# Optimization experiments

Hardware: AMD Instinct MI355X
Metric: run time of the kernel (lower is better)

## Reference

```python
import jax, jax.numpy as jnp
import numpy as np

B = 32768
W = 7            # window_size (fixed: classifier head outputs 7*2 -> view(B, 7, 2))
F = 80           # per-frame feature size
WF = W * F       # window_feature_size = 560
EH = 512         # encoder_hidden_size
EO = 512         # encoder_output_size
H = 512          # core_hidden_size
NUM_STEPS = 7
EPS = 1e-5

def _linear(x, w, b):
    return x @ w.T + b

def _bn(x, g, bt, m, v):
    # BatchNorm1d in eval mode (running stats)
    return (x - m) * g / jnp.sqrt(v + EPS) + bt

def _ln(x, g, b):
    mu = x.mean(-1, keepdims=True)
    var = x.var(-1, keepdims=True)
    return (x - mu) / jnp.sqrt(var + EPS) * g + b

def setup_inputs():
    key = jax.random.key(0)
    ks = iter(jax.random.split(key, 40))
    def rn(shape, s=0.05):
        return jax.random.normal(next(ks), shape, dtype=jnp.float32) * s
    def rv(shape):
        return jax.random.uniform(next(ks), shape, dtype=jnp.float32) + 0.5
    return {
        'features': jax.random.normal(next(ks), (B, W, F), dtype=jnp.float32),
        'dec_w': rn((W, H)), 'dec_b': rn((W,)),
        'dec_bn_g': rv((W,)), 'dec_bn_b': rn((W,)), 'dec_bn_m': rn((W,)), 'dec_bn_v': rv((W,)),
        'ea1_w': rn((EH, W)), 'ea1_b': rn((EH,)),
        'ea1_bn_g': rv((EH,)), 'ea1_bn_b': rn((EH,)), 'ea1_bn_m': rn((EH,)), 'ea1_bn_v': rv((EH,)),
        'ea2_w': rn((EO, EH)), 'ea2_b': rn((EO,)),
        'ea2_bn_g': rv((EO,)), 'ea2_bn_b': rn((EO,)), 'ea2_bn_m': rn((EO,)), 'ea2_bn_v': rv((EO,)),
        'ei1_w': rn((EH, WF)), 'ei1_b': rn((EH,)),
        'ei1_bn_g': rv((EH,)), 'ei1_bn_b': rn((EH,)), 'ei1_bn_m': rn((EH,)), 'ei1_bn_v': rv((EH,)),
        'ei2_w': rn((EO, EH)), 'ei2_b': rn((EO,)),
        'ei2_bn_g': rv((EO,)), 'ei2_bn_b': rn((EO,)), 'ei2_bn_m': rn((EO,)), 'ei2_bn_v': rv((EO,)),
        'w_ih': rn((4 * H, EO)), 'w_hh': rn((4 * H, H)), 'b_ih': rn((4 * H,)), 'b_hh': rn((4 * H,)),
        'ln_g': rv((H,)), 'ln_b': rn((H,)),
        'cls_w': rn((2 * W, H)), 'cls_b': rn((2 * W,)),
    }

def _forward(features, dec_w, dec_b, dec_bn_g, dec_bn_b, dec_bn_m, dec_bn_v,
             ea1_w, ea1_b, ea1_bn_g, ea1_bn_b, ea1_bn_m, ea1_bn_v,
             ea2_w, ea2_b, ea2_bn_g, ea2_bn_b, ea2_bn_m, ea2_bn_v,
             ei1_w, ei1_b, ei1_bn_g, ei1_bn_b, ei1_bn_m, ei1_bn_v,
             ei2_w, ei2_b, ei2_bn_g, ei2_bn_b, ei2_bn_m, ei2_bn_v,
             w_ih, w_hh, b_ih, b_hh, ln_g, ln_b, cls_w, cls_b):
    Bsz = features.shape[0]

    def encoder(att):
        # attention branch: Linear -> BN -> ReLU -> Linear -> BN
        a = jax.nn.relu(_bn(_linear(att, ea1_w, ea1_b), ea1_bn_g, ea1_bn_b, ea1_bn_m, ea1_bn_v))
        a = _bn(_linear(a, ea2_w, ea2_b), ea2_bn_g, ea2_bn_b, ea2_bn_m, ea2_bn_v)
        # attended-input branch on flattened (features * att)
        ai = (features * att[:, :, None]).reshape(Bsz, WF)
        x = jax.nn.relu(_bn(_linear(ai, ei1_w, ei1_b), ei1_bn_g, ei1_bn_b, ei1_bn_m, ei1_bn_v))
        x = _bn(_linear(x, ei2_w, ei2_b), ei2_bn_g, ei2_bn_b, ei2_bn_m, ei2_bn_v)
        return jax.nn.relu(a + x)

    def lstm_step(x, h, c):
        gates = x @ w_ih.T + b_ih + h @ w_hh.T + b_hh  # [B, 4H], torch gate order i,f,g,o
        i, f, g, o = jnp.split(gates, 4, axis=-1)
        c = jax.nn.sigmoid(f) * c + jax.nn.sigmoid(i) * jnp.tanh(g)
        h = jax.nn.sigmoid(o) * jnp.tanh(c)
        return h, c

    # initial pass: uniform attention, zero LSTM state (state=None -> no LN)
    att0 = jnp.full((Bsz, W), 1.0 / W, dtype=features.dtype)
    h, c = lstm_step(encoder(att0), jnp.zeros((Bsz, H), features.dtype), jnp.zeros((Bsz, H), features.dtype))

    def body(carry, _):
        h, c = carry
        # decoder: Linear -> BN -> smooth softmax
        logits = _bn(_linear(h, dec_w, dec_b), dec_bn_g, dec_bn_b, dec_bn_m, dec_bn_v)
        s = jax.nn.sigmoid(logits)
        att = s / s.sum(-1, keepdims=True)
        agg = encoder(att)
        hn, cn = lstm_step(agg, _ln(h, ln_g, ln_b), _ln(c, ln_g, ln_b))
        return (hn, cn), None

    (h, c), _ = jax.lax.scan(body, (h, c), None, length=NUM_STEPS)
    out = _linear(h, cls_w, cls_b).reshape(Bsz, W, 2)
    return jax.nn.log_softmax(out, axis=2)

def reference(features, dec_w, dec_b, dec_bn_g, dec_bn_b, dec_bn_m, dec_bn_v,
              ea1_w, ea1_b, ea1_bn_g, ea1_bn_b, ea1_bn_m, ea1_bn_v,
              ea2_w, ea2_b, ea2_bn_g, ea2_bn_b, ea2_bn_m, ea2_bn_v,
              ei1_w, ei1_b, ei1_bn_g, ei1_bn_b, ei1_bn_m, ei1_bn_v,
              ei2_w, ei2_b, ei2_bn_g, ei2_bn_b, ei2_bn_m, ei2_bn_v,
              w_ih, w_hh, b_ih, b_hh, ln_g, ln_b, cls_w, cls_b):
    return _forward(features, dec_w, dec_b, dec_bn_g, dec_bn_b, dec_bn_m, dec_bn_v,
                    ea1_w, ea1_b, ea1_bn_g, ea1_bn_b, ea1_bn_m, ea1_bn_v,
                    ea2_w, ea2_b, ea2_bn_g, ea2_bn_b, ea2_bn_m, ea2_bn_v,
                    ei1_w, ei1_b, ei1_bn_g, ei1_bn_b, ei1_bn_m, ei1_bn_v,
                    ei2_w, ei2_b, ei2_bn_g, ei2_bn_b, ei2_bn_m, ei2_bn_v,
                    w_ih, w_hh, b_ih, b_hh, ln_g, ln_b, cls_w, cls_b)
```

## Files before the change

kernel.cpp:

```cpp
#include <hip/hip_runtime.h>
#include <cstdint>
#include <cstddef>

#define BSZ 32768
#define WN 7
#define WF 560
#define K1P 576
#define EPS 1e-5f

typedef __attribute__((ext_vector_type(8))) short bf16x8;
typedef __attribute__((ext_vector_type(4))) float f32x4;

__device__ __forceinline__ float b2f(short s) {
  union { float f; unsigned u; } x; x.u = ((unsigned)(unsigned short)s) << 16; return x.f;
}
__device__ __forceinline__ short f2b(float f) {
  union { float f; unsigned u; } x; x.f = f;
  unsigned r = x.u + 0x7fffu + ((x.u >> 16) & 1u);
  return (short)(r >> 16);
}
__device__ __forceinline__ float sigf(float x) { return 1.0f / (1.0f + __expf(-x)); }
__device__ __forceinline__ float ftanh(float x) {
  float t = __expf(-2.0f * fabsf(x));
  float r = (1.0f - t) / (1.0f + t);
  return copysignf(r, x);
}

__device__ __forceinline__ void async_copy16(const short* g, short* l) {
  __builtin_amdgcn_global_load_lds((const __attribute__((address_space(1))) unsigned*)g,
                                   (__attribute__((address_space(3))) unsigned*)l, 16, 0, 0);
}


__global__ void fold_small_k(const float* __restrict__ dec_w, const float* __restrict__ dec_b,
                             const float* __restrict__ dec_g, const float* __restrict__ dec_bt,
                             const float* __restrict__ dec_m, const float* __restrict__ dec_v,
                             const float* __restrict__ ea1_w, const float* __restrict__ ea1_b,
                             const float* __restrict__ ea1_g, const float* __restrict__ ea1_bt,
                             const float* __restrict__ ea1_m, const float* __restrict__ ea1_v,
                             float* __restrict__ decwf, float* __restrict__ decb8,
                             float* __restrict__ ea1f)
{
  int t = blockIdx.x * 256 + threadIdx.x;
  if (t < 7 * 512) {
    int w = t >> 9;
    float s = dec_g[w] * rsqrtf(dec_v[w] + EPS);
    decwf[t] = dec_w[t] * s;
  }
  if (t < 8) {
    if (t < 7) {
      float s = dec_g[t] * rsqrtf(dec_v[t] + EPS);
      decb8[t] = (dec_b[t] - dec_m[t]) * s + dec_bt[t];
    } else decb8[t] = 0.0f;
  }
  if (t < 512) {
    float s = ea1_g[t] * rsqrtf(ea1_v[t] + EPS);
    #pragma unroll
    for (int w = 0; w < 7; ++w) ea1f[t * 8 + w] = ea1_w[t * 7 + w] * s;
    ea1f[t * 8 + 7] = (ea1_b[t] - ea1_m[t]) * s + ea1_bt[t];
  }
}

__global__ void fold_ei1_k(const float* __restrict__ w, const float* __restrict__ b,
                           const float* __restrict__ g, const float* __restrict__ bt,
                           const float* __restrict__ m, const float* __restrict__ v,
                           short* __restrict__ ei1f, float* __restrict__ bias1)
{
  int idx = blockIdx.x * 256 + threadIdx.x;
  int n = idx / K1P, k = idx % K1P;
  float s = g[n] * rsqrtf(v[n] + EPS);
  ei1f[idx] = (k < WF) ? f2b(w[n * WF + k] * s) : (short)0;
  if (k == 0) bias1[n] = (b[n] - m[n]) * s + bt[n];
}

__global__ void fold_w2_k(const float* __restrict__ wi, const float* __restrict__ bi,
                          const float* __restrict__ gi, const float* __restrict__ bti,
                          const float* __restrict__ mi, const float* __restrict__ vi,
                          const float* __restrict__ wa, const float* __restrict__ ba,
                          const float* __restrict__ ga, const float* __restrict__ bta,
                          const float* __restrict__ ma, const float* __restrict__ va,
                          short* __restrict__ W2, float* __restrict__ bias2)
{
  int idx = blockIdx.x * 256 + threadIdx.x;
  int n = idx >> 10, k = idx & 1023;
  float si = gi[n] * rsqrtf(vi[n] + EPS);
  float sa = ga[n] * rsqrtf(va[n] + EPS);
  float val = (k < 512) ? wi[n * 512 + k] * si : wa[n * 512 + (k - 512)] * sa;
  W2[idx] = f2b(val);
  if (k == 0)
    bias2[n] = (bi[n] - mi[n]) * si + bti[n] + (ba[n] - ma[n]) * sa + bta[n];
}

__global__ void fold_wg_k(const float* __restrict__ w_ih, const float* __restrict__ w_hh,
                          const float* __restrict__ b_ih, const float* __restrict__ b_hh,
                          short* __restrict__ Wg, float* __restrict__ biasg)
{
  int idx = blockIdx.x * 256 + threadIdx.x;
  int c = idx >> 10, k = idx & 1023;
  int g = (c >> 4) & 3;
  int u = (c >> 6) * 16 + (c & 15);
  int r = g * 512 + u;
  float val = (k < 512) ? w_ih[r * 512 + k] : w_hh[r * 512 + (k - 512)];
  Wg[idx] = f2b(val);
  if (k == 0) biasg[c] = b_ih[r] + b_hh[r];
}

__global__ __launch_bounds__(512)
void attln_k(const float* __restrict__ hbuf, const float* __restrict__ cbuf,
             const float* __restrict__ decwf, const float* __restrict__ decb8,
             const float* __restrict__ ea1f,
             const float* __restrict__ ln_g, const float* __restrict__ ln_b,
             const float* __restrict__ feat,
             short* __restrict__ ghA, short* __restrict__ c_ln,
             short* __restrict__ xa, short* __restrict__ ai, int init)
{
  const int lane = threadIdx.x & 63;
  const int b = blockIdx.x * 8 + (threadIdx.x >> 6);
  float av[WN];
  if (init) {
    const float c7 = 1.0f / 7.0f;
    #pragma unroll
    for (int w = 0; w < WN; ++w) av[w] = c7;
    int4 z = make_int4(0, 0, 0, 0);
    *(int4*)&ghA[b * 1024 + 512 + lane * 8] = z;
    *(int4*)&c_ln[b * 512 + lane * 8] = z;
  } else {
    float hl[8];
    const float* hp = hbuf + (size_t)b * 512 + lane * 8;
    *(float4*)&hl[0] = *(const float4*)hp;
    *(float4*)&hl[4] = *(const float4*)(hp + 4);
    float s = 0.f, s2 = 0.f;
    #pragma unroll
    for (int e = 0; e < 8; ++e) { s += hl[e]; s2 += hl[e] * hl[e]; }
    float p[WN];
    #pragma unroll
    for (int w = 0; w < WN; ++w) {
      const float* dw = decwf + w * 512 + lane * 8;
      float4 w0 = *(const float4*)dw, w1 = *(const float4*)(dw + 4);
      p[w] = hl[0] * w0.x + hl[1] * w0.y + hl[2] * w0.z + hl[3] * w0.w
           + hl[4] * w1.x + hl[5] * w1.y + hl[6] * w1.z + hl[7] * w1.w;
    }
    #pragma unroll
    for (int o = 32; o > 0; o >>= 1) {
      s  += __shfl_xor(s, o);
      s2 += __shfl_xor(s2, o);
      #pragma unroll
      for (int w = 0; w < WN; ++w) p[w] += __shfl_xor(p[w], o);
    }
    float mu = s * (1.0f / 512.0f);
    float var = s2 * (1.0f / 512.0f) - mu * mu;
    float rstd = rsqrtf(var + EPS);
    float ssum = 0.f;
    #pragma unroll
    for (int w = 0; w < WN; ++w) { float sg = sigf(p[w] + decb8[w]); av[w] = sg; ssum += sg; }
    float inv = 1.0f / ssum;
    #pragma unroll
    for (int w = 0; w < WN; ++w) av[w] *= inv;
    short o8[8];
    #pragma unroll
    for (int e = 0; e < 8; ++e) {
      int i = lane * 8 + e;
      o8[e] = f2b((hl[e] - mu) * rstd * ln_g[i] + ln_b[i]);
    }
    *(int4*)&ghA[b * 1024 + 512 + lane * 8] = *(int4*)o8;
    float cl[8];
    const float* cp = cbuf + (size_t)b * 512 + lane * 8;
    *(float4*)&cl[0] = *(const float4*)cp;
    *(float4*)&cl[4] = *(const float4*)(cp + 4);
    float cs = 0.f, cs2 = 0.f;
    #pragma unroll
    for (int e = 0; e < 8; ++e) { cs += cl[e]; cs2 += cl[e] * cl[e]; }
    #pragma unroll
    for (int o = 32; o > 0; o >>= 1) {
      cs  += __shfl_xor(cs, o);
      cs2 += __shfl_xor(cs2, o);
    }
    float cmu = cs * (1.0f / 512.0f);
    float cvar = cs2 * (1.0f / 512.0f) - cmu * cmu;
    float crstd = rsqrtf(cvar + EPS);
    #pragma unroll
    for (int e = 0; e < 8; ++e) {
      int i = lane * 8 + e;
      o8[e] = f2b((cl[e] - cmu) * crstd * ln_g[i] + ln_b[i]);
    }
    *(int4*)&c_ln[b * 512 + lane * 8] = *(int4*)o8;
  }
  short a8[8];
  #pragma unroll
  for (int e = 0; e < 8; ++e) {
    int n = lane * 8 + e;
    const float* wr = ea1f + n * 8;
    float4 w0 = *(const float4*)wr, w1 = *(const float4*)(wr + 4);
    float v = w1.w
            + av[0] * w0.x + av[1] * w0.y + av[2] * w0.z + av[3] * w0.w
            + av[4] * w1.x + av[5] * w1.y + av[6] * w1.z;
    a8[e] = f2b(fmaxf(v, 0.0f));
  }
  *(int4*)&xa[b * 1024 + 512 + lane * 8] = *(int4*)a8;
  const float* fr = feat + (size_t)b * WF;
  short* air = ai + (size_t)b * K1P;
  #pragma unroll
  for (int rr = 0; rr < 2; ++rr) {
    int c8 = lane + rr * 64;
    if (c8 < 72) {
      int k = c8 * 8;
      short s8[8];
      if (k < WF) {
        int window = c8 / 10;
        float a = av[0];
        #pragma unroll
        for (int w = 1; w < WN; ++w) a = (window == w) ? av[w] : a;
        float4 f0 = *(const float4*)(fr + k);
        float4 f1 = *(const float4*)(fr + k + 4);
        s8[0] = f2b(f0.x * a); s8[1] = f2b(f0.y * a); s8[2] = f2b(f0.z * a); s8[3] = f2b(f0.w * a);
        s8[4] = f2b(f1.x * a); s8[5] = f2b(f1.y * a); s8[6] = f2b(f1.z * a); s8[7] = f2b(f1.w * a);
      } else {
        #pragma unroll
        for (int e = 0; e < 8; ++e) s8[e] = 0;
      }
      *(int4*)&air[k] = *(int4*)s8;
    }
  }
}

#define STAGE128(SRC, LD, K0, S) do {                                          \
    _Pragma("unroll")                                                          \
    for (int r_ = 0; r_ < 4; ++r_) {                                           \
      int idx_ = r_ * 256 + t;                                                 \
      int row_ = idx_ >> 3, dcol_ = (idx_ & 7) * 8;                            \
      int scol_ = dcol_ ^ ((row_ & 7) << 3);                                   \
      async_copy16(SRC + (size_t)row_ * (LD) + (K0) + scol_, &S[idx_ * 8]);    \
    }                                                                          \
  } while (0)

#define READ_FRAG(S, ROW, KS) \
  (*(const bf16x8*)&S[(ROW) * 64 + (((KS)) ^ (((ROW) & 7) << 3))])

__global__ __launch_bounds__(256)
void gemm_bt_k(const short* __restrict__ A, int lda,
               const short* __restrict__ Wt, int K,
               const float* __restrict__ bias,
               short* __restrict__ C, int ldc)
{
  const int bswz = blockIdx.x;
  const int xcd = bswz & 7, slot = bswz >> 3;
  const int m0 = (xcd + 8 * (slot >> 2)) * 128;
  const int n0 = (slot & 3) * 128;
  __shared__ short sA[128 * 64];
  __shared__ short sB[128 * 64];
  const int t = threadIdx.x;
  const int wv = t >> 6, lane = t & 63;
  const int wm = (wv & 1) * 64, wn = (wv >> 1) * 64;
  const int lr = lane & 15, lk = (lane >> 4) * 8;

  f32x4 acc[4][4] = {};
  const short* Ab = A + (size_t)m0 * lda;
  const short* Wb = Wt + (size_t)n0 * K;

  for (int k0 = 0; k0 < K; k0 += 64) {
    STAGE128(Ab, lda, k0, sA);
    STAGE128(Wb, K, k0, sB);
    __syncthreads();
    #pragma unroll
    for (int ks = 0; ks < 64; ks += 32) {
      bf16x8 af[4], bfr[4];
      #pragma unroll
      for (int i = 0; i < 4; ++i) af[i]  = READ_FRAG(sA, wm + i * 16 + lr, ks + lk);
      #pragma unroll
      for (int j = 0; j < 4; ++j) bfr[j] = READ_FRAG(sB, wn + j * 16 + lr, ks + lk);
      #pragma unroll
      for (int i = 0; i < 4; ++i)
        #pragma unroll
        for (int j = 0; j < 4; ++j)
          acc[i][j] = __builtin_amdgcn_mfma_f32_16x16x32_bf16(af[i], bfr[j], acc[i][j], 0, 0, 0);
    }
    __syncthreads();
  }
  #pragma unroll
  for (int j = 0; j < 4; ++j) {
    int col = n0 + wn + j * 16 + lr;
    float bs = bias[col];
    #pragma unroll
    for (int i = 0; i < 4; ++i) {
      int rbase = m0 + wm + i * 16 + (lane >> 4) * 4;
      #pragma unroll
      for (int e = 0; e < 4; ++e) {
        float v = acc[i][j][e] + bs;
        C[(size_t)(rbase + e) * ldc + col] = f2b(fmaxf(v, 0.0f));
      }
    }
  }
}


#define GS_STAGE(g) do {                                                             \
    short* dA_ = &sA[((g) & 1) * 16384];                                             \
    short* dB_ = &sB[((g) & 1) * 16384];                                             \
    _Pragma("unroll")                                                                \
    for (int q_ = 0; q_ < 4; ++q_) {                                                 \
      int idx_ = q_ * 512 + t;                                                       \
      int row_ = idx_ >> 3, ds_ = idx_ & 7;                                          \
      int sc_ = (ds_ ^ (row_ & 7)) * 8;                                              \
      async_copy16(A + (size_t)(m0 + row_) * 1024 + (g) * 64 + sc_, dA_ + idx_ * 8); \
    }                                                                                \
    _Pragma("unroll")                                                                \
    for (int q_ = 0; q_ < 4; ++q_) {                                                 \
      int idx_ = q_ * 512 + t;                                                       \
      int row_ = idx_ >> 3, ds_ = idx_ & 7;                                          \
      int sc_ = (ds_ ^ (row_ & 7)) * 8;                                              \
      async_copy16(Wg + (size_t)(n0 + row_) * 1024 + (g) * 64 + sc_, dB_ + idx_ * 8);\
    }                                                                                \
  } while (0)

#define GS_COMPUTE(g) do {                                                           \
    const short* bA_ = &sA[((g) & 1) * 16384];                                       \
    const short* bB_ = &sB[((g) & 1) * 16384];                                       \
    _Pragma("unroll")                                                                \
    for (int ks_ = 0; ks_ < 2; ++ks_) {                                              \
      bf16x8 af_[4], bf_[8];                                                         \
      _Pragma("unroll")                                                              \
      for (int mf_ = 0; mf_ < 4; ++mf_) {                                            \
        int row_ = wm * 64 + mf_ * 16 + lr;                                          \
        af_[mf_] = *(const bf16x8*)&bA_[row_ * 64 + (((ks_ * 4 + hi) ^ (row_ & 7)) * 8)]; \
      }                                                                              \
      _Pragma("unroll")                                                              \
      for (int nf_ = 0; nf_ < 8; ++nf_) {                                            \
        int row_ = wn * 128 + nf_ * 16 + lr;                                         \
        bf_[nf_] = *(const bf16x8*)&bB_[row_ * 64 + (((ks_ * 4 + hi) ^ (row_ & 7)) * 8)]; \
      }                                                                              \
      __builtin_amdgcn_s_setprio(1);                                                 \
      _Pragma("unroll")                                                              \
      for (int mf_ = 0; mf_ < 4; ++mf_)                                              \
        _Pragma("unroll")                                                            \
        for (int nf_ = 0; nf_ < 8; ++nf_)                                            \
          acc[mf_][nf_] = __builtin_amdgcn_mfma_f32_16x16x32_bf16(af_[mf_], bf_[nf_], acc[mf_][nf_], 0, 0, 0); \
      __builtin_amdgcn_s_setprio(0);                                                 \
    }                                                                                \
  } while (0)

__global__ __launch_bounds__(512, 2)
void gates_k(const short* __restrict__ A,
             const short* __restrict__ Wg,
             const float* __restrict__ biasg,
             const short* __restrict__ c_ln,
             float* __restrict__ hbuf, float* __restrict__ cbuf)
{
  __shared__ short sA[2 * 256 * 64];
  __shared__ short sB[2 * 256 * 64];
  const int m0 = blockIdx.x * 256;
  const int n0 = blockIdx.y * 256;
  const int t = threadIdx.x;
  const int wid = t >> 6, lane = t & 63;
  const int wm = wid >> 1, wn = wid & 1;
  const int lr = lane & 15, hi = lane >> 4;

  f32x4 acc[4][8] = {};

  GS_STAGE(0);
  asm volatile("s_waitcnt vmcnt(0)" ::: "memory");
  __builtin_amdgcn_s_barrier();

  #pragma unroll
  for (int g = 0; g < 16; ++g) {
    if (g + 1 < 16) GS_STAGE(g + 1);
    GS_COMPUTE(g);
    if (g + 1 < 16) {
      asm volatile("s_waitcnt vmcnt(0) lgkmcnt(0)" ::: "memory");
      __builtin_amdgcn_s_barrier();
    }
  }

  #pragma unroll
  for (int grp = 0; grp < 2; ++grp) {
    const int cb = n0 + wn * 128 + grp * 64;
    const int u = ((cb >> 6)) * 16 + lr;
    const float bi_ = biasg[cb + 0 * 16 + lr];
    const float bf2 = biasg[cb + 1 * 16 + lr];
    const float bg_ = biasg[cb + 2 * 16 + lr];
    const float bo_ = biasg[cb + 3 * 16 + lr];
    #pragma unroll
    for (int mf = 0; mf < 4; ++mf) {
      int rbase = m0 + wm * 64 + mf * 16 + hi * 4;
      #pragma unroll
      for (int e = 0; e < 4; ++e) {
        int row = rbase + e;
        float iv = sigf(acc[mf][grp * 4 + 0][e] + bi_);
        float fv = sigf(acc[mf][grp * 4 + 1][e] + bf2);
        float gv = ftanh(acc[mf][grp * 4 + 2][e] + bg_);
        float ov = sigf(acc[mf][grp * 4 + 3][e] + bo_);
        float cold = b2f(c_ln[(size_t)row * 512 + u]);
        float cc = fv * cold + iv * gv;
        hbuf[(size_t)row * 512 + u] = ov * ftanh(cc);
        cbuf[(size_t)row * 512 + u] = cc;
      }
    }
  }
}

__global__ __launch_bounds__(512)
void cls_k(const float* __restrict__ hbuf, const float* __restrict__ cw,
           const float* __restrict__ cb, float* __restrict__ out)
{
  const int lane = threadIdx.x & 63;
  const int b = blockIdx.x * 8 + (threadIdx.x >> 6);
  float hl[8];
  const float* hp = hbuf + (size_t)b * 512 + lane * 8;
  *(float4*)&hl[0] = *(const float4*)hp;
  *(float4*)&hl[4] = *(const float4*)(hp + 4);
  float p[14];
  #pragma unroll
  for (int tcol = 0; tcol < 14; ++tcol) {
    const float* wr = cw + tcol * 512 + lane * 8;
    float4 w0 = *(const float4*)wr, w1 = *(const float4*)(wr + 4);
    p[tcol] = hl[0] * w0.x + hl[1] * w0.y + hl[2] * w0.z + hl[3] * w0.w
            + hl[4] * w1.x + hl[5] * w1.y + hl[6] * w1.z + hl[7] * w1.w;
  }
  #pragma unroll
  for (int o = 32; o > 0; o >>= 1)
    #pragma unroll
    for (int tcol = 0; tcol < 14; ++tcol) p[tcol] += __shfl_xor(p[tcol], o);
  if (lane < 14) {
    float z = cb[lane];
    #pragma unroll
    for (int tcol = 0; tcol < 14; ++tcol) if (lane == tcol) z += p[tcol];
    float zp = __shfl_xor(z, 1);
    float m = fmaxf(z, zp);
    float l = m + __logf(__expf(z - m) + __expf(zp - m));
    out[(size_t)b * 14 + lane] = z - l;
  }
}


extern "C" void kernel_launch(void* const* d_in, const int* in_sizes, int n_in,
                              void* d_out, int out_size, void* d_ws, size_t ws_size,
                              hipStream_t stream)
{
  const float* features = (const float*)d_in[0];
  const float* dec_w    = (const float*)d_in[1];
  const float* dec_b    = (const float*)d_in[2];
  const float* dec_bn_g = (const float*)d_in[3];
  const float* dec_bn_b = (const float*)d_in[4];
  const float* dec_bn_m = (const float*)d_in[5];
  const float* dec_bn_v = (const float*)d_in[6];
  const float* ea1_w    = (const float*)d_in[7];
  const float* ea1_b    = (const float*)d_in[8];
  const float* ea1_bn_g = (const float*)d_in[9];
  const float* ea1_bn_b = (const float*)d_in[10];
  const float* ea1_bn_m = (const float*)d_in[11];
  const float* ea1_bn_v = (const float*)d_in[12];
  const float* ea2_w    = (const float*)d_in[13];
  const float* ea2_b    = (const float*)d_in[14];
  const float* ea2_bn_g = (const float*)d_in[15];
  const float* ea2_bn_b = (const float*)d_in[16];
  const float* ea2_bn_m = (const float*)d_in[17];
  const float* ea2_bn_v = (const float*)d_in[18];
  const float* ei1_w    = (const float*)d_in[19];
  const float* ei1_b    = (const float*)d_in[20];
  const float* ei1_bn_g = (const float*)d_in[21];
  const float* ei1_bn_b = (const float*)d_in[22];
  const float* ei1_bn_m = (const float*)d_in[23];
  const float* ei1_bn_v = (const float*)d_in[24];
  const float* ei2_w    = (const float*)d_in[25];
  const float* ei2_b    = (const float*)d_in[26];
  const float* ei2_bn_g = (const float*)d_in[27];
  const float* ei2_bn_b = (const float*)d_in[28];
  const float* ei2_bn_m = (const float*)d_in[29];
  const float* ei2_bn_v = (const float*)d_in[30];
  const float* w_ih     = (const float*)d_in[31];
  const float* w_hh     = (const float*)d_in[32];
  const float* b_ih     = (const float*)d_in[33];
  const float* b_hh     = (const float*)d_in[34];
  const float* ln_g     = (const float*)d_in[35];
  const float* ln_b     = (const float*)d_in[36];
  const float* cls_w    = (const float*)d_in[37];
  const float* cls_b    = (const float*)d_in[38];
  (void)in_sizes; (void)n_in; (void)out_size;

  int chunk = BSZ;
  while (chunk > 2048 && (size_t)chunk * 10368 + (16u << 20) > ws_size) chunk >>= 1;

  char* ws = (char*)d_ws;
  size_t off = 0;
  auto carve = [&](size_t bytes) -> void* {
    void* p = ws + off;
    off += (bytes + 255) & ~(size_t)255;
    return p;
  };
  short* ei1f  = (short*)carve((size_t)512 * K1P * 2);
  float* bias1 = (float*)carve(512 * 4);
  short* W2    = (short*)carve((size_t)512 * 1024 * 2);
  float* bias2 = (float*)carve(512 * 4);
  short* Wg    = (short*)carve((size_t)2048 * 1024 * 2);
  float* biasg = (float*)carve(2048 * 4);
  float* decwf = (float*)carve(7 * 512 * 4);
  float* decb8 = (float*)carve(8 * 4);
  float* ea1f  = (float*)carve(512 * 8 * 4);
  float* hbuf  = (float*)carve((size_t)chunk * 512 * 4);
  float* cbuf  = (float*)carve((size_t)chunk * 512 * 4);
  short* ghA   = (short*)carve((size_t)chunk * 1024 * 2);
  short* xa    = (short*)carve((size_t)chunk * 1024 * 2);
  short* clnb  = (short*)carve((size_t)chunk * 512 * 2);
  short* ai    = (short*)carve((size_t)chunk * K1P * 2);

  fold_small_k<<<16, 256, 0, stream>>>(dec_w, dec_b, dec_bn_g, dec_bn_b, dec_bn_m, dec_bn_v,
                                       ea1_w, ea1_b, ea1_bn_g, ea1_bn_b, ea1_bn_m, ea1_bn_v,
                                       decwf, decb8, ea1f);
  fold_ei1_k<<<(512 * K1P) / 256, 256, 0, stream>>>(ei1_w, ei1_b, ei1_bn_g, ei1_bn_b,
                                                    ei1_bn_m, ei1_bn_v, ei1f, bias1);
  fold_w2_k<<<(512 * 1024) / 256, 256, 0, stream>>>(ei2_w, ei2_b, ei2_bn_g, ei2_bn_b, ei2_bn_m, ei2_bn_v,
                                                    ea2_w, ea2_b, ea2_bn_g, ea2_bn_b, ea2_bn_m, ea2_bn_v,
                                                    W2, bias2);
  fold_wg_k<<<(2048 * 1024) / 256, 256, 0, stream>>>(w_ih, w_hh, b_ih, b_hh, Wg, biasg);

  for (int base = 0; base < BSZ; base += chunk) {
    const float* featc = features + (size_t)base * WF;
    float* outc = (float*)d_out + (size_t)base * 14;
    for (int s = 0; s < 8; ++s) {
      attln_k<<<chunk / 8, 512, 0, stream>>>(hbuf, cbuf, decwf, decb8, ea1f, ln_g, ln_b,
                                             featc, ghA, clnb, xa, ai, (s == 0) ? 1 : 0);
      gemm_bt_k<<<(chunk / 128) * 4, 256, 0, stream>>>(ai, K1P, ei1f, K1P, bias1, xa, 1024);
      gemm_bt_k<<<(chunk / 128) * 4, 256, 0, stream>>>(xa, 1024, W2, 1024, bias2, ghA, 1024);
      gates_k<<<dim3(chunk / 256, 8), 512, 0, stream>>>(ghA, Wg, biasg, clnb, hbuf, cbuf);
    }
    cls_k<<<chunk / 8, 512, 0, stream>>>(hbuf, cls_w, cls_b, outc);
  }
}
```

Baseline: 2.765 ms.

## Interleave B-fragment LDS loads with MFMA quarters in gates GEMM loop

Restructures the gates GEMM inner loop so that each K-tile is computed in four N-quarters. B fragments for the next quarter are double-buffered in registers and loaded from LDS while the current quarter's MFMAs run, and extra barriers are inserted between quarters. The goal is to hide LDS read latency behind matrix-core work and to spread LDS traffic across waves. In exchange it adds barriers per tile, which can add sync overhead and register pressure.

```diff
diff --git a/kernel.cpp b/kernel.cpp
--- a/kernel.cpp
+++ b/kernel.cpp
@@ -312,29 +312,13 @@
     }                                                                                \
   } while (0)
 
-#define GS_COMPUTE(g) do {                                                           \
-    const short* bA_ = &sA[((g) & 1) * 16384];                                       \
-    const short* bB_ = &sB[((g) & 1) * 16384];                                       \
+#define GS_LOADB(BUF, DST, NQ) do {                                                  \
     _Pragma("unroll")                                                                \
-    for (int ks_ = 0; ks_ < 2; ++ks_) {                                              \
-      bf16x8 af_[4], bf_[8];                                                         \
+    for (int nfi_ = 0; nfi_ < 2; ++nfi_) {                                           \
+      int row_ = wn * 128 + (NQ) * 32 + nfi_ * 16 + lr;                              \
       _Pragma("unroll")                                                              \
-      for (int mf_ = 0; mf_ < 4; ++mf_) {                                            \
-        int row_ = wm * 64 + mf_ * 16 + lr;                                          \
-        af_[mf_] = *(const bf16x8*)&bA_[row_ * 64 + (((ks_ * 4 + hi) ^ (row_ & 7)) * 8)]; \
-      }                                                                              \
-      _Pragma("unroll")                                                              \
-      for (int nf_ = 0; nf_ < 8; ++nf_) {                                            \
-        int row_ = wn * 128 + nf_ * 16 + lr;                                         \
-        bf_[nf_] = *(const bf16x8*)&bB_[row_ * 64 + (((ks_ * 4 + hi) ^ (row_ & 7)) * 8)]; \
-      }                                                                              \
-      __builtin_amdgcn_s_setprio(1);                                                 \
-      _Pragma("unroll")                                                              \
-      for (int mf_ = 0; mf_ < 4; ++mf_)                                              \
-        _Pragma("unroll")                                                            \
-        for (int nf_ = 0; nf_ < 8; ++nf_)                                            \
-          acc[mf_][nf_] = __builtin_amdgcn_mfma_f32_16x16x32_bf16(af_[mf_], bf_[nf_], acc[mf_][nf_], 0, 0, 0); \
-      __builtin_amdgcn_s_setprio(0);                                                 \
+      for (int ks_ = 0; ks_ < 2; ++ks_)                                              \
+        DST[nfi_][ks_] = *(const bf16x8*)&BUF[row_ * 64 + (((ks_ * 4 + hi) ^ (row_ & 7)) * 8)]; \
     }                                                                                \
   } while (0)
 
@@ -362,12 +346,45 @@
 
   #pragma unroll
   for (int g = 0; g < 16; ++g) {
+    const short* bA_ = &sA[(g & 1) * 16384];
+    const short* bB_ = &sB[(g & 1) * 16384];
     if (g + 1 < 16) GS_STAGE(g + 1);
-    GS_COMPUTE(g);
-    if (g + 1 < 16) {
-      asm volatile("s_waitcnt vmcnt(0) lgkmcnt(0)" ::: "memory");
+
+    bf16x8 af_[4][2];
+    #pragma unroll
+    for (int mf_ = 0; mf_ < 4; ++mf_) {
+      int row_ = wm * 64 + mf_ * 16 + lr;
+      #pragma unroll
+      for (int ks_ = 0; ks_ < 2; ++ks_)
+        af_[mf_][ks_] = *(const bf16x8*)&bA_[row_ * 64 + (((ks_ * 4 + hi) ^ (row_ & 7)) * 8)];
+    }
+    bf16x8 b0[2][2], b1[2][2];
+    GS_LOADB(bB_, b0, 0);
+
+    #pragma unroll
+    for (int q = 0; q < 4; ++q) {
       __builtin_amdgcn_s_barrier();
-    }
+      __builtin_amdgcn_s_setprio(1);
+      #pragma unroll
+      for (int mf_ = 0; mf_ < 4; ++mf_)
+        #pragma unroll
+        for (int nfi_ = 0; nfi_ < 2; ++nfi_) {
+          if (q & 1) {
+            acc[mf_][q * 2 + nfi_] = __builtin_amdgcn_mfma_f32_16x16x32_bf16(af_[mf_][0], b1[nfi_][0], acc[mf_][q * 2 + nfi_], 0, 0, 0);
+            acc[mf_][q * 2 + nfi_] = __builtin_amdgcn_mfma_f32_16x16x32_bf16(af_[mf_][1], b1[nfi_][1], acc[mf_][q * 2 + nfi_], 0, 0, 0);
+          } else {
+            acc[mf_][q * 2 + nfi_] = __builtin_amdgcn_mfma_f32_16x16x32_bf16(af_[mf_][0], b0[nfi_][0], acc[mf_][q * 2 + nfi_], 0, 0, 0);
+            acc[mf_][q * 2 + nfi_] = __builtin_amdgcn_mfma_f32_16x16x32_bf16(af_[mf_][1], b0[nfi_][1], acc[mf_][q * 2 + nfi_], 0, 0, 0);
+          }
+        }
+      __builtin_amdgcn_s_setprio(0);
+      if (q == 0) GS_LOADB(bB_, b1, 1);
+      else if (q == 1) GS_LOADB(bB_, b0, 2);
+      else if (q == 2) GS_LOADB(bB_, b1, 3);
+      else if (g + 1 < 16)
+        asm volatile("s_waitcnt vmcnt(0)" ::: "memory");
+    }
+    __builtin_amdgcn_s_barrier();
   }
 
   #pragma unroll
```

Result: no change. 2.783 ms (+0.7%).

## Double-buffer LDS tiles in encoder GEMM to overlap loads with MFMA

Applied to the files above, without the earlier changes.

The encoder GEMM now uses two LDS buffers for A and B, issuing the async copies for the next K-tile before computing on the current one. It then waits on vmcnt and a barrier before the next iteration. The K trip count becomes a template parameter so the loop fully unrolls. The aim is to hide global-memory latency behind MFMA work. In exchange LDS use doubles to 64KB per block, which may reduce occupancy, and the unroll raises code size.

```diff
diff --git a/kernel.cpp b/kernel.cpp
--- a/kernel.cpp
+++ b/kernel.cpp
@@ -223,19 +223,30 @@
   }
 }
 
-#define STAGE128(SRC, LD, K0, S) do {                                          \
-    _Pragma("unroll")                                                          \
-    for (int r_ = 0; r_ < 4; ++r_) {                                           \
-      int idx_ = r_ * 256 + t;                                                 \
-      int row_ = idx_ >> 3, dcol_ = (idx_ & 7) * 8;                            \
-      int scol_ = dcol_ ^ ((row_ & 7) << 3);                                   \
-      async_copy16(SRC + (size_t)row_ * (LD) + (K0) + scol_, &S[idx_ * 8]);    \
-    }                                                                          \
+
+#define E_STAGE(g) do {                                                              \
+    short* dA_ = &sA[((g) & 1) * 8192];                                              \
+    short* dB_ = &sB[((g) & 1) * 8192];                                              \
+    _Pragma("unroll")                                                                \
+    for (int q_ = 0; q_ < 4; ++q_) {                                                 \
+      int idx_ = q_ * 256 + t;                                                       \
+      int row_ = idx_ >> 3, dcol_ = (idx_ & 7) * 8;                                  \
+      int scol_ = dcol_ ^ ((row_ & 7) << 3);                                         \
+      async_copy16(Ab + (size_t)row_ * lda + (g) * 64 + scol_, dA_ + idx_ * 8);      \
+    }                                                                                \
+    _Pragma("unroll")                                                                \
+    for (int q_ = 0; q_ < 4; ++q_) {                                                 \
+      int idx_ = q_ * 256 + t;                                                       \
+      int row_ = idx_ >> 3, dcol_ = (idx_ & 7) * 8;                                  \
+      int scol_ = dcol_ ^ ((row_ & 7) << 3);                                         \
+      async_copy16(Wb + (size_t)row_ * K + (g) * 64 + scol_, dB_ + idx_ * 8);        \
+    }                                                                                \
   } while (0)
 
-#define READ_FRAG(S, ROW, KS) \
-  (*(const bf16x8*)&S[(ROW) * 64 + (((KS)) ^ (((ROW) & 7) << 3))])
-
+#define READ_FRAGB(BASE, ROW, KS) \
+  (*(const bf16x8*)&BASE[(ROW) * 64 + (((KS)) ^ (((ROW) & 7) << 3))])
+
+template<int KT>
 __global__ __launch_bounds__(256)
 void gemm_bt_k(const short* __restrict__ A, int lda,
                const short* __restrict__ Wt, int K,
@@ -246,8 +257,8 @@
   const int xcd = bswz & 7, slot = bswz >> 3;
   const int m0 = (xcd + 8 * (slot >> 2)) * 128;
   const int n0 = (slot & 3) * 128;
-  __shared__ short sA[128 * 64];
-  __shared__ short sB[128 * 64];
+  __shared__ short sA[2 * 128 * 64];
+  __shared__ short sB[2 * 128 * 64];
   const int t = threadIdx.x;
   const int wv = t >> 6, lane = t & 63;
   const int wm = (wv & 1) * 64, wn = (wv >> 1) * 64;
@@ -257,24 +268,32 @@
   const short* Ab = A + (size_t)m0 * lda;
   const short* Wb = Wt + (size_t)n0 * K;
 
-  for (int k0 = 0; k0 < K; k0 += 64) {
-    STAGE128(Ab, lda, k0, sA);
-    STAGE128(Wb, K, k0, sB);
-    __syncthreads();
+  E_STAGE(0);
+  asm volatile("s_waitcnt vmcnt(0)" ::: "memory");
+  __builtin_amdgcn_s_barrier();
+
+  #pragma unroll
+  for (int g = 0; g < KT; ++g) {
+    const short* bA_ = &sA[(g & 1) * 8192];
+    const short* bB_ = &sB[(g & 1) * 8192];
+    if (g + 1 < KT) E_STAGE(g + 1);
     #pragma unroll
     for (int ks = 0; ks < 64; ks += 32) {
       bf16x8 af[4], bfr[4];
       #pragma unroll
-      for (int i = 0; i < 4; ++i) af[i]  = READ_FRAG(sA, wm + i * 16 + lr, ks + lk);
+      for (int i = 0; i < 4; ++i) af[i]  = READ_FRAGB(bA_, wm + i * 16 + lr, ks + lk);
       #pragma unroll
-      for (int j = 0; j < 4; ++j) bfr[j] = READ_FRAG(sB, wn + j * 16 + lr, ks + lk);
+      for (int j = 0; j < 4; ++j) bfr[j] = READ_FRAGB(bB_, wn + j * 16 + lr, ks + lk);
       #pragma unroll
       for (int i = 0; i < 4; ++i)
         #pragma unroll
         for (int j = 0; j < 4; ++j)
           acc[i][j] = __builtin_amdgcn_mfma_f32_16x16x32_bf16(af[i], bfr[j], acc[i][j], 0, 0, 0);
     }
-    __syncthreads();
+    if (g + 1 < KT) {
+      asm volatile("s_waitcnt vmcnt(0)" ::: "memory");
+      __builtin_amdgcn_s_barrier();
+    }
   }
   #pragma unroll
   for (int j = 0; j < 4; ++j) {
@@ -518,8 +537,8 @@
     for (int s = 0; s < 8; ++s) {
       attln_k<<<chunk / 8, 512, 0, stream>>>(hbuf, cbuf, decwf, decb8, ea1f, ln_g, ln_b,
                                              featc, ghA, clnb, xa, ai, (s == 0) ? 1 : 0);
-      gemm_bt_k<<<(chunk / 128) * 4, 256, 0, stream>>>(ai, K1P, ei1f, K1P, bias1, xa, 1024);
-      gemm_bt_k<<<(chunk / 128) * 4, 256, 0, stream>>>(xa, 1024, W2, 1024, bias2, ghA, 1024);
+      gemm_bt_k<9><<<(chunk / 128) * 4, 256, 0, stream>>>(ai, K1P, ei1f, K1P, bias1, xa, 1024);
+      gemm_bt_k<16><<<(chunk / 128) * 4, 256, 0, stream>>>(xa, 1024, W2, 1024, bias2, ghA, 1024);
       gates_k<<<dim3(chunk / 256, 8), 512, 0, stream>>>(ghA, Wg, biasg, clnb, hbuf, cbuf);
     }
     cls_k<<<chunk / 8, 512, 0, stream>>>(hbuf, cls_w, cls_b, outc);
```

New measurement: 2.689 ms. 1.03x faster.
